# Optimization experiments

Measured on AMD Instinct MI355X. Metric: run time of the kernel, lower is better.

## Reference

```python
import jax, jax.numpy as jnp
import numpy as np
import math

N_AGENTS = 16

def _mlp2(x, W1, b1, W2, b2):
    # tanh on first layer only, matching the torch module
    return jnp.tanh(x @ W1 + b1) @ W2 + b2

def setup_inputs() -> dict:
    key = jax.random.key(0)
    ks = jax.random.split(key, 24)
    B, N, A, IN, D = 2048, N_AGENTS, 32, 128, 128
    NODES = B * N
    s = 0.05
    inp = {
        "obs": jax.random.normal(ks[0], (NODES, IN), jnp.float32),
        "policies": jax.random.uniform(ks[1], (NODES, A), jnp.float32),
        "actions": jax.random.uniform(ks[2], (NODES, A), jnp.float32),
        "weights": jax.random.uniform(ks[3], (1,), jnp.float32),
        "noise": jax.random.normal(ks[4], (NODES, N, A), jnp.float32) * 0.1,
        "Wk1": jax.random.normal(ks[5], (IN, 32), jnp.float32) * s,
        "bk1": jnp.zeros((32,), jnp.float32),
        "Wk2": jax.random.normal(ks[6], (32, D), jnp.float32) * s,
        "bk2": jnp.zeros((D,), jnp.float32),
        "Wq1": jax.random.normal(ks[7], (IN, 32), jnp.float32) * s,
        "bq1": jnp.zeros((32,), jnp.float32),
        "Wq2": jax.random.normal(ks[8], (32, D), jnp.float32) * s,
        "bq2": jnp.zeros((D,), jnp.float32),
        "Wv1": jax.random.normal(ks[9], (IN, 32), jnp.float32) * s,
        "bv1": jnp.zeros((32,), jnp.float32),
        "Wv2": jax.random.normal(ks[10], (32, D), jnp.float32) * s,
        "bv2": jnp.zeros((D,), jnp.float32),
        "Wval": jax.random.normal(ks[11], (D + A, 1), jnp.float32) * s,
        "bval": jnp.zeros((1,), jnp.float32),
    }
    return inp

def reference(obs, policies, actions, weights, noise,
              Wk1, bk1, Wk2, bk2, Wq1, bq1, Wq2, bq2, Wv1, bv1, Wv2, bv2,
              Wval, bval):
    N = N_AGENTS
    NODES, _ = obs.shape
    B = NODES // N
    A = policies.shape[-1]
    D = Wk2.shape[1]

    # ---- SoftAttentionInput: graph soft attention over complete N-agent graphs
    k = _mlp2(obs, Wk1, bk1, Wk2, bk2).reshape(B, N, D)
    q = _mlp2(obs, Wq1, bq1, Wq2, bq2).reshape(B, N, D)
    v = _mlp2(obs, Wv1, bv1, Wv2, bv2).reshape(B, N, D)
    # score for receiver i from sender j: key[j] . query[i]
    scores = jnp.einsum('bjd,bid->bij', k, q) / math.sqrt(D)
    alpha = jax.nn.softmax(scores, axis=-1)               # softmax over senders j
    obs_proc = jnp.einsum('bij,bjd->bid', alpha, v)       # [B,N,D]

    # ---- SoftAttentionWeight: PRD mixing of policies and noisy actions
    pi = policies.reshape(B, N, A)
    act = actions.reshape(B, N, A)
    w = weights                                           # scalar mixing weight, shape (1,)
    # z[b,i,k] = w*act[b,k] + (1-w)*pi[b,k] + noise (mailbox of receiver i)
    z = w * act[:, None, :, :] + (1.0 - w) * pi[:, None, :, :] + noise.reshape(B, N, N, A)
    # place_policies construction: z_final[b,i,j,k] = pi[b,k] if k==j else z[b,i,k];
    # mean over k  =>  (pi[b,j] - z[b,i,j] + sum_k z[b,i,k]) / N
    z_sum = jnp.sum(z, axis=2)                            # [B,N,A]
    z_mix = (pi[:, None, :, :] - z + z_sum[:, :, None, :]) / N  # [B,i,j,A]

    obs_b = jnp.broadcast_to(obs_proc[:, None, :, :], (B, N, N, D))  # [b,i,j] = obs_proc[b,j]
    obs_final = jnp.concatenate([obs_b, z_mix], axis=-1).reshape(B * N, N, D + A)

    # ---- ValueNetwork
    x = obs_final @ Wval + bval                           # [B*N, N, 1]
    weights_preproc = alpha.reshape(B * N, N, 1)
    return x, weights_preproc
```

## Files before the change

kernel.cpp:

```cpp
#include <hip/hip_runtime.h>

typedef __attribute__((ext_vector_type(8))) short bf16x8;
typedef __attribute__((ext_vector_type(4))) float f32x4;

__device__ __forceinline__ unsigned short f2bf(float f){
  union { float f; unsigned int u; } v; v.f = f;
  unsigned int u = v.u;
  return (unsigned short)((u + 0x7FFFu + ((u >> 16) & 1u)) >> 16);
}

__device__ __forceinline__ float fast_tanh(float x){
  x = fminf(15.f, fmaxf(-15.f, x));
  float e = __expf(2.f * x);
  return (e - 1.f) / (e + 1.f);
}

__device__ __forceinline__ float dot128(const float* __restrict__ a,
                                        const float* __restrict__ b){
  float s = 0.f;
  for (int c = 0; c < 128; c += 4){
    float4 x = *(const float4*)(a + c);
    float4 y = *(const float4*)(b + c);
    s += x.x*y.x + x.y*y.y + x.z*y.z + x.w*y.w;
  }
  return s;
}

#define GRPSUM(x) { x += __shfl_xor(x, 1); x += __shfl_xor(x, 2); \
                    x += __shfl_xor(x, 4); x += __shfl_xor(x, 8); }

__global__ __launch_bounds__(64) void k0_kernel(
    const float* __restrict__ Wk1, const float* __restrict__ Wq1, const float* __restrict__ Wv1,
    const float* __restrict__ Wk2, const float* __restrict__ bk2,
    const float* __restrict__ Wq2, const float* __restrict__ bq2,
    const float* __restrict__ Wv2, const float* __restrict__ bv2,
    const float* __restrict__ Wval, float* __restrict__ ws)
{
  const int tid = blockIdx.x * 64 + threadIdx.x;
  const float rs = 0.08838834764831845f;
  unsigned short* bp = (unsigned short*)ws;
  unsigned short* b2 = (unsigned short*)(ws + 6144);

  if (tid < 1536){
    const int e = tid & 7, l = (tid >> 3) & 63, tt = tid >> 9;
    const int g = (l >> 4) * 8 + e;
    float val = 0.f;
    if (tt < 2){
      const int h = (l & 15) + tt * 16;
      val = rs * dot128(Wk2 + h * 128, Wq2 + g * 128);
    } else if ((l & 15) == 0){
      val = rs * dot128(Wq2 + g * 128, bk2);
    }
    b2[tid] = f2bf(val);
  } else if (tid < 1600){
    const int h = tid - 1536;
    if (h < 32) ws[6912 + h] = rs * dot128(Wk2 + h * 128, bq2);
    else        ws[6944 + (h - 32)] = dot128(Wv2 + (h - 32) * 128, Wval);
  } else if (tid == 1600){
    ws[6976] = rs * dot128(bk2, bq2);
  } else if (tid == 1601){
    ws[6977] = dot128(bv2, Wval);
  }

  for (int idx = tid; idx < 12288; idx += 4096){
    const int e  = idx & 7;
    const int l  = (idx >> 3) & 63;
    const int kc = (idx >> 9) & 3;
    const int nt = (idx >> 11) & 1;
    const int m  = idx >> 12;
    const float* W1 = (m == 0) ? Wk1 : ((m == 1) ? Wq1 : Wv1);
    const int krow = kc * 32 + (l >> 4) * 8 + e;
    const int col  = nt * 16 + (l & 15);
    bp[idx] = f2bf(W1[krow * 32 + col]);
  }
}

__global__ __launch_bounds__(256) void k1_kernel(
    const float* __restrict__ obs, const float* __restrict__ noise,
    const float* __restrict__ bk1p, const float* __restrict__ bq1p, const float* __restrict__ bv1p,
    const float* __restrict__ Wval, const float* __restrict__ ws,
    float* __restrict__ out_x, float* __restrict__ out_alpha,
    float* __restrict__ ws_ov, int BA)
{
  __shared__ __align__(16) unsigned short hk_s[4][512];
  __shared__ __align__(16) unsigned short hq_s[4][512];
  __shared__ __align__(16) unsigned short tq_s[4][512];
  __shared__ __align__(16) float rql_s[4][16];
  __shared__ __align__(16) float vvl_s[4][16];
  __shared__ float nvw[256];

  const int t = threadIdx.x;

  if ((int)blockIdx.x >= BA){
    const int b = blockIdx.x - BA;
    const int q = t & 7;
    const float4 wv4 = *(const float4*)(Wval + 128 + q * 4);
    const float* nb = noise + (size_t)b * 8192 + (t >> 3) * 32 + q * 4;
#pragma unroll
    for (int p = 0; p < 8; p++){
      float4 n4 = *(const float4*)(nb + p * 1024);
      float s = n4.x*wv4.x + n4.y*wv4.y + n4.z*wv4.z + n4.w*wv4.w;
      s += __shfl_xor(s, 1); s += __shfl_xor(s, 2); s += __shfl_xor(s, 4);
      if (q == 0) nvw[p * 32 + (t >> 3)] = s;
    }
    __syncthreads();
    out_x[(size_t)b * 256 + t] = nvw[t];
    return;
  }

  const int wid = t >> 6, l = t & 63;
  const int b = blockIdx.x * 4 + wid;
  const int li = l & 15, gp = l >> 4;

  const float* orow = obs + (size_t)(b * 16 + li) * 128 + gp * 8;
  bf16x8 afr[4];
#pragma unroll
  for (int kc = 0; kc < 4; kc++){
    float4 x0 = *(const float4*)(orow + kc * 32);
    float4 x1 = *(const float4*)(orow + kc * 32 + 4);
    bf16x8 a;
    a[0]=(short)f2bf(x0.x); a[1]=(short)f2bf(x0.y); a[2]=(short)f2bf(x0.z); a[3]=(short)f2bf(x0.w);
    a[4]=(short)f2bf(x1.x); a[5]=(short)f2bf(x1.y); a[6]=(short)f2bf(x1.z); a[7]=(short)f2bf(x1.w);
    afr[kc] = a;
  }
  const bf16x8* bp  = (const bf16x8*)ws;
  const bf16x8* b2p = (const bf16x8*)(ws + 6144);
  const bf16x8 b20 = b2p[l], b21 = b2p[64 + l], b22 = b2p[128 + l];
  const float u0 = ws[6912 + li], u1 = ws[6928 + li];
  const float wv0 = ws[6944 + li], wv1 = ws[6960 + li];
  const float ccv = ws[6976], cvv = ws[6977];
  const float bk0 = bk1p[li], bk1v = bk1p[16 + li];
  const float bq0 = bq1p[li], bq1v = bq1p[16 + li];
  const float bv0 = bv1p[li], bv1v = bv1p[16 + li];

  f32x4 acc[6];
#pragma unroll
  for (int mt = 0; mt < 6; mt++){ f32x4 z = {0.f,0.f,0.f,0.f}; acc[mt] = z; }
#pragma unroll
  for (int mt = 0; mt < 6; mt++){
#pragma unroll
    for (int kc = 0; kc < 4; kc++)
      acc[mt] = __builtin_amdgcn_mfma_f32_16x16x32_bf16(afr[kc], bp[(mt*4+kc)*64 + l], acc[mt], 0, 0, 0);
  }

  unsigned short* hkb = hk_s[wid];
  unsigned short* hqb = hq_s[wid];
#pragma unroll
  for (int tile = 0; tile < 2; tile++){
    const float bk_ = tile ? bk1v : bk0;
    const float bq_ = tile ? bq1v : bq0;
    f32x4 ck = acc[tile], cq = acc[2 + tile];
#pragma unroll
    for (int r = 0; r < 4; r++){
      hkb[(gp*4+r)*32 + tile*16 + li] = f2bf(fast_tanh(ck[r] + bk_));
      hqb[(gp*4+r)*32 + tile*16 + li] = f2bf(fast_tanh(cq[r] + bq_));
    }
  }

  {
    f32x4 c0 = acc[4], c1 = acc[5];
    float vp0 = wv0*fast_tanh(c0[0]+bv0) + wv1*fast_tanh(c1[0]+bv1v);
    float vp1 = wv0*fast_tanh(c0[1]+bv0) + wv1*fast_tanh(c1[1]+bv1v);
    float vp2 = wv0*fast_tanh(c0[2]+bv0) + wv1*fast_tanh(c1[2]+bv1v);
    float vp3 = wv0*fast_tanh(c0[3]+bv0) + wv1*fast_tanh(c1[3]+bv1v);
    GRPSUM(vp0); GRPSUM(vp1); GRPSUM(vp2); GRPSUM(vp3);
    if (li == 0){
      float4 vq; vq.x = vp0+cvv; vq.y = vp1+cvv; vq.z = vp2+cvv; vq.w = vp3+cvv;
      *(float4*)&vvl_s[wid][gp*4] = vq;
    }
  }

  const bf16x8 aq = *(const bf16x8*)(hqb + li*32 + gp*8);
  f32x4 cu0 = {u0,u0,u0,u0}, cu1 = {u1,u1,u1,u1}, cu2 = {ccv,ccv,ccv,ccv};
  f32x4 tq0 = __builtin_amdgcn_mfma_f32_16x16x32_bf16(aq, b20, cu0, 0, 0, 0);
  f32x4 tq1 = __builtin_amdgcn_mfma_f32_16x16x32_bf16(aq, b21, cu1, 0, 0, 0);
  f32x4 rqt = __builtin_amdgcn_mfma_f32_16x16x32_bf16(aq, b22, cu2, 0, 0, 0);
  if (li == 0){
    float4 rv; rv.x = rqt[0]; rv.y = rqt[1]; rv.z = rqt[2]; rv.w = rqt[3];
    *(float4*)&rql_s[wid][gp*4] = rv;
  }
  unsigned short* tqb = tq_s[wid];
#pragma unroll
  for (int r = 0; r < 4; r++){
    tqb[(gp*4+r)*32 + li]      = f2bf(tq0[r]);
    tqb[(gp*4+r)*32 + 16 + li] = f2bf(tq1[r]);
  }

  const bf16x8 ak = *(const bf16x8*)(hkb + li*32 + gp*8);
  const bf16x8 bt = *(const bf16x8*)(tqb + li*32 + gp*8);
  f32x4 zz = {0.f,0.f,0.f,0.f};
  f32x4 S = __builtin_amdgcn_mfma_f32_16x16x32_bf16(ak, bt, zz, 0, 0, 0);
  const float rc = rql_s[wid][li];
  float s0 = S[0]+rc, s1 = S[1]+rc, s2 = S[2]+rc, s3 = S[3]+rc;

  float mx = fmaxf(fmaxf(s0, s1), fmaxf(s2, s3));
  mx = fmaxf(mx, __shfl_xor(mx, 16)); mx = fmaxf(mx, __shfl_xor(mx, 32));
  float e0 = __expf(s0-mx), e1 = __expf(s1-mx), e2 = __expf(s2-mx), e3 = __expf(s3-mx);
  float sm = e0+e1+e2+e3;
  sm += __shfl_xor(sm, 16); sm += __shfl_xor(sm, 32);
  const float inv = 1.f / sm;
  const float a0 = e0*inv, a1 = e1*inv, a2 = e2*inv, a3 = e3*inv;

  float* aT = (float*)tqb;
  { float4 av4; av4.x = a0; av4.y = a1; av4.z = a2; av4.w = a3;
    *(float4*)&aT[li*16 + gp*4] = av4; }
  { float4 o4 = *(const float4*)&aT[l*4];
    *(float4*)(out_alpha + (size_t)b*256 + l*4) = o4; }

  float4 vq4 = *(const float4*)&vvl_s[wid][gp*4];
  float ovp = a0*vq4.x + a1*vq4.y + a2*vq4.z + a3*vq4.w;
  ovp += __shfl_xor(ovp, 16); ovp += __shfl_xor(ovp, 32);
  if (l < 16) ws_ov[(size_t)b*16 + l] = ovp;
}

__global__ __launch_bounds__(256) void kc_kernel(
    const float* __restrict__ policies, const float* __restrict__ actions,
    const float* __restrict__ weights, const float* __restrict__ Wval,
    const float* __restrict__ bval, const float* __restrict__ ws_ov,
    float* __restrict__ out_x)
{
  __shared__ float pv_l[16], av_l[16];
  const int b = blockIdx.x, t = threadIdx.x;
  const float w = weights[0];
  {
    const int j = t >> 4; const int a0 = (t & 15) * 2;
    const float wa = Wval[128 + a0], wb = Wval[129 + a0];
    const float* pp = policies + ((size_t)(b * 16 + j)) * 32 + a0;
    const float* ap = actions  + ((size_t)(b * 16 + j)) * 32 + a0;
    float p = pp[0]*wa + pp[1]*wb;
    float a = ap[0]*wa + ap[1]*wb;
    GRPSUM(p); GRPSUM(a);
    if ((t & 15) == 0){ pv_l[j] = p; av_l[j] = a; }
  }
  __syncthreads();
  const int j = t & 15;
  const float pv = pv_l[j], av = av_l[j];
  const float nv = out_x[(size_t)b * 256 + t];
  const float zval = w * av + (1.f - w) * pv + nv;
  float zs = zval;
  GRPSUM(zs);
  out_x[(size_t)b * 256 + t] = ws_ov[(size_t)b * 16 + j] + (pv - zval + zs) * 0.0625f + bval[0];
}

extern "C" void kernel_launch(void* const* d_in, const int* in_sizes, int n_in,
                              void* d_out, int out_size, void* d_ws, size_t ws_size,
                              hipStream_t stream)
{
  const float* obs      = (const float*)d_in[0];
  const float* policies = (const float*)d_in[1];
  const float* actions  = (const float*)d_in[2];
  const float* weights  = (const float*)d_in[3];
  const float* noise    = (const float*)d_in[4];
  const float* Wk1  = (const float*)d_in[5];
  const float* bk1  = (const float*)d_in[6];
  const float* Wk2  = (const float*)d_in[7];
  const float* bk2  = (const float*)d_in[8];
  const float* Wq1  = (const float*)d_in[9];
  const float* bq1  = (const float*)d_in[10];
  const float* Wq2  = (const float*)d_in[11];
  const float* bq2  = (const float*)d_in[12];
  const float* Wv1  = (const float*)d_in[13];
  const float* bv1  = (const float*)d_in[14];
  const float* Wv2  = (const float*)d_in[15];
  const float* bv2  = (const float*)d_in[16];
  const float* Wval = (const float*)d_in[17];
  const float* bval = (const float*)d_in[18];

  float* out = (float*)d_out;
  float* ws  = (float*)d_ws;
  float* ws_ov = ws + 7168;

  const int NODES = in_sizes[0] / 128;
  const int B = NODES / 16;
  const int BA = B / 4;

  float* out_x     = out;
  float* out_alpha = out + (size_t)NODES * 16;

  hipLaunchKernelGGL(k0_kernel, dim3(64), dim3(64), 0, stream,
                     Wk1, Wq1, Wv1, Wk2, bk2, Wq2, bq2, Wv2, bv2, Wval, ws);
  hipLaunchKernelGGL(k1_kernel, dim3(BA + B), dim3(256), 0, stream,
                     obs, noise, bk1, bq1, bv1, Wval, ws,
                     out_x, out_alpha, ws_ov, BA);
  hipLaunchKernelGGL(kc_kernel, dim3(B), dim3(256), 0, stream,
                     policies, actions, weights, Wval, bval, ws_ov, out_x);
}
```

Before: 31.36 us.

## Fuse noise projection and PRD mixing into the attention kernel

Merges the separate noise-projection blocks and the final mixing kernel into the attention kernel. Each wave now handles one batch end to end: it streams that batch's noise in four software-pipelined register chunks interleaved with the MFMA work, computes the policy and action projections, and writes out_x directly. This drops one kernel launch and the global round trips through out_x and ws_ov. In exchange, register pressure is much higher (two 8-float4 noise buffers) and the grid falls to B/4 blocks, with launch bounds raised to ask for 2 blocks per CU.

```diff
diff --git a/kernel.cpp b/kernel.cpp
--- a/kernel.cpp
+++ b/kernel.cpp
@@ -75,54 +75,53 @@
   }
 }
 
-__global__ __launch_bounds__(256) void k1_kernel(
-    const float* __restrict__ obs, const float* __restrict__ noise,
+__global__ __launch_bounds__(256, 2) void fused_kernel(
+    const float* __restrict__ obs,
+    const float* __restrict__ policies, const float* __restrict__ actions,
+    const float* __restrict__ noise, const float* __restrict__ weights,
     const float* __restrict__ bk1p, const float* __restrict__ bq1p, const float* __restrict__ bv1p,
-    const float* __restrict__ Wval, const float* __restrict__ ws,
-    float* __restrict__ out_x, float* __restrict__ out_alpha,
-    float* __restrict__ ws_ov, int BA)
+    const float* __restrict__ Wval, const float* __restrict__ bval,
+    const float* __restrict__ ws,
+    float* __restrict__ out_x, float* __restrict__ out_alpha)
 {
   __shared__ __align__(16) unsigned short hk_s[4][512];
   __shared__ __align__(16) unsigned short hq_s[4][512];
   __shared__ __align__(16) unsigned short tq_s[4][512];
   __shared__ __align__(16) float rql_s[4][16];
   __shared__ __align__(16) float vvl_s[4][16];
-  __shared__ float nvw[256];
+  __shared__ __align__(16) float nvw_s[4][256];
+  __shared__ __align__(16) float pvl_s[4][16], avl_s[4][16], ovl_s[4][16];
 
   const int t = threadIdx.x;
-
-  if ((int)blockIdx.x >= BA){
-    const int b = blockIdx.x - BA;
-    const int q = t & 7;
-    const float4 wv4 = *(const float4*)(Wval + 128 + q * 4);
-    const float* nb = noise + (size_t)b * 8192 + (t >> 3) * 32 + q * 4;
-#pragma unroll
-    for (int p = 0; p < 8; p++){
-      float4 n4 = *(const float4*)(nb + p * 1024);
-      float s = n4.x*wv4.x + n4.y*wv4.y + n4.z*wv4.z + n4.w*wv4.w;
-      s += __shfl_xor(s, 1); s += __shfl_xor(s, 2); s += __shfl_xor(s, 4);
-      if (q == 0) nvw[p * 32 + (t >> 3)] = s;
-    }
-    __syncthreads();
-    out_x[(size_t)b * 256 + t] = nvw[t];
-    return;
-  }
-
   const int wid = t >> 6, l = t & 63;
   const int b = blockIdx.x * 4 + wid;
   const int li = l & 15, gp = l >> 4;
 
   const float* orow = obs + (size_t)(b * 16 + li) * 128 + gp * 8;
-  bf16x8 afr[4];
+  float4 ob[8];
 #pragma unroll
   for (int kc = 0; kc < 4; kc++){
-    float4 x0 = *(const float4*)(orow + kc * 32);
-    float4 x1 = *(const float4*)(orow + kc * 32 + 4);
-    bf16x8 a;
-    a[0]=(short)f2bf(x0.x); a[1]=(short)f2bf(x0.y); a[2]=(short)f2bf(x0.z); a[3]=(short)f2bf(x0.w);
-    a[4]=(short)f2bf(x1.x); a[5]=(short)f2bf(x1.y); a[6]=(short)f2bf(x1.z); a[7]=(short)f2bf(x1.w);
-    afr[kc] = a;
-  }
+    ob[kc * 2]     = *(const float4*)(orow + kc * 32);
+    ob[kc * 2 + 1] = *(const float4*)(orow + kc * 32 + 4);
+  }
+
+  const int q8 = l & 7, r8 = l >> 3;
+  const float* nb = noise + (size_t)b * 8192 + r8 * 32 + q8 * 4;
+  float4 nzA[8], nzB[8];
+#pragma unroll
+  for (int p = 0; p < 8; p++) nzA[p] = *(const float4*)(nb + p * 256);
+
+  const int jp = l >> 2, seg = l & 3;
+  const float* pp = policies + (size_t)(b * 16 + jp) * 32 + seg * 8;
+  const float* ap = actions  + (size_t)(b * 16 + jp) * 32 + seg * 8;
+  float4 pA0 = *(const float4*)(pp);
+  float4 pA1 = *(const float4*)(pp + 4);
+  float4 aA0 = *(const float4*)(ap);
+  float4 aA1 = *(const float4*)(ap + 4);
+  const float4 wpa = *(const float4*)(Wval + 128 + seg * 8);
+  const float4 wpb = *(const float4*)(Wval + 132 + seg * 8);
+  const float4 wv4 = *(const float4*)(Wval + 128 + q8 * 4);
+
   const bf16x8* bp  = (const bf16x8*)ws;
   const bf16x8* b2p = (const bf16x8*)(ws + 6144);
   const bf16x8 b20 = b2p[l], b21 = b2p[64 + l], b22 = b2p[128 + l];
@@ -132,7 +131,19 @@
   const float bk0 = bk1p[li], bk1v = bk1p[16 + li];
   const float bq0 = bq1p[li], bq1v = bq1p[16 + li];
   const float bv0 = bv1p[li], bv1v = bv1p[16 + li];
-
+  const float wscal = weights[0];
+  const float bvs = bval[0];
+
+  bf16x8 afr[4];
+#pragma unroll
+  for (int kc = 0; kc < 4; kc++){
+    bf16x8 a;
+    a[0]=(short)f2bf(ob[kc*2].x); a[1]=(short)f2bf(ob[kc*2].y);
+    a[2]=(short)f2bf(ob[kc*2].z); a[3]=(short)f2bf(ob[kc*2].w);
+    a[4]=(short)f2bf(ob[kc*2+1].x); a[5]=(short)f2bf(ob[kc*2+1].y);
+    a[6]=(short)f2bf(ob[kc*2+1].z); a[7]=(short)f2bf(ob[kc*2+1].w);
+    afr[kc] = a;
+  }
   f32x4 acc[6];
 #pragma unroll
   for (int mt = 0; mt < 6; mt++){ f32x4 z = {0.f,0.f,0.f,0.f}; acc[mt] = z; }
@@ -170,6 +181,18 @@
     }
   }
 
+#pragma unroll
+  for (int p = 0; p < 8; p++) nzB[p] = *(const float4*)(nb + 2048 + p * 256);
+  float* nvw = nvw_s[wid];
+#pragma unroll
+  for (int p = 0; p < 8; p++){
+    float s = nzA[p].x*wv4.x + nzA[p].y*wv4.y + nzA[p].z*wv4.z + nzA[p].w*wv4.w;
+    s += __shfl_xor(s, 1); s += __shfl_xor(s, 2); s += __shfl_xor(s, 4);
+    if (q8 == 0) nvw[p * 8 + r8] = s;
+  }
+#pragma unroll
+  for (int p = 0; p < 8; p++) nzA[p] = *(const float4*)(nb + 4096 + p * 256);
+
   const bf16x8 aq = *(const bf16x8*)(hqb + li*32 + gp*8);
   f32x4 cu0 = {u0,u0,u0,u0}, cu1 = {u1,u1,u1,u1}, cu2 = {ccv,ccv,ccv,ccv};
   f32x4 tq0 = __builtin_amdgcn_mfma_f32_16x16x32_bf16(aq, b20, cu0, 0, 0, 0);
@@ -210,36 +233,61 @@
   float4 vq4 = *(const float4*)&vvl_s[wid][gp*4];
   float ovp = a0*vq4.x + a1*vq4.y + a2*vq4.z + a3*vq4.w;
   ovp += __shfl_xor(ovp, 16); ovp += __shfl_xor(ovp, 32);
-  if (l < 16) ws_ov[(size_t)b*16 + l] = ovp;
-}
-
-__global__ __launch_bounds__(256) void kc_kernel(
-    const float* __restrict__ policies, const float* __restrict__ actions,
-    const float* __restrict__ weights, const float* __restrict__ Wval,
-    const float* __restrict__ bval, const float* __restrict__ ws_ov,
-    float* __restrict__ out_x)
-{
-  __shared__ float pv_l[16], av_l[16];
-  const int b = blockIdx.x, t = threadIdx.x;
-  const float w = weights[0];
+  if (l < 16) ovl_s[wid][li] = ovp;
+
+#pragma unroll
+  for (int p = 0; p < 8; p++){
+    float s = nzB[p].x*wv4.x + nzB[p].y*wv4.y + nzB[p].z*wv4.z + nzB[p].w*wv4.w;
+    s += __shfl_xor(s, 1); s += __shfl_xor(s, 2); s += __shfl_xor(s, 4);
+    if (q8 == 0) nvw[64 + p * 8 + r8] = s;
+  }
+#pragma unroll
+  for (int p = 0; p < 8; p++) nzB[p] = *(const float4*)(nb + 6144 + p * 256);
+
   {
-    const int j = t >> 4; const int a0 = (t & 15) * 2;
-    const float wa = Wval[128 + a0], wb = Wval[129 + a0];
-    const float* pp = policies + ((size_t)(b * 16 + j)) * 32 + a0;
-    const float* ap = actions  + ((size_t)(b * 16 + j)) * 32 + a0;
-    float p = pp[0]*wa + pp[1]*wb;
-    float a = ap[0]*wa + ap[1]*wb;
-    GRPSUM(p); GRPSUM(a);
-    if ((t & 15) == 0){ pv_l[j] = p; av_l[j] = a; }
-  }
-  __syncthreads();
-  const int j = t & 15;
-  const float pv = pv_l[j], av = av_l[j];
-  const float nv = out_x[(size_t)b * 256 + t];
-  const float zval = w * av + (1.f - w) * pv + nv;
-  float zs = zval;
-  GRPSUM(zs);
-  out_x[(size_t)b * 256 + t] = ws_ov[(size_t)b * 16 + j] + (pv - zval + zs) * 0.0625f + bval[0];
+    float pvv = pA0.x*wpa.x + pA0.y*wpa.y + pA0.z*wpa.z + pA0.w*wpa.w
+              + pA1.x*wpb.x + pA1.y*wpb.y + pA1.z*wpb.z + pA1.w*wpb.w;
+    float avv = aA0.x*wpa.x + aA0.y*wpa.y + aA0.z*wpa.z + aA0.w*wpa.w
+              + aA1.x*wpb.x + aA1.y*wpb.y + aA1.z*wpb.z + aA1.w*wpb.w;
+    pvv += __shfl_xor(pvv, 1); pvv += __shfl_xor(pvv, 2);
+    avv += __shfl_xor(avv, 1); avv += __shfl_xor(avv, 2);
+    if (seg == 0){ pvl_s[wid][jp] = pvv; avl_s[wid][jp] = avv; }
+  }
+
+#pragma unroll
+  for (int p = 0; p < 8; p++){
+    float s = nzA[p].x*wv4.x + nzA[p].y*wv4.y + nzA[p].z*wv4.z + nzA[p].w*wv4.w;
+    s += __shfl_xor(s, 1); s += __shfl_xor(s, 2); s += __shfl_xor(s, 4);
+    if (q8 == 0) nvw[128 + p * 8 + r8] = s;
+  }
+#pragma unroll
+  for (int p = 0; p < 8; p++){
+    float s = nzB[p].x*wv4.x + nzB[p].y*wv4.y + nzB[p].z*wv4.z + nzB[p].w*wv4.w;
+    s += __shfl_xor(s, 1); s += __shfl_xor(s, 2); s += __shfl_xor(s, 4);
+    if (q8 == 0) nvw[192 + p * 8 + r8] = s;
+  }
+
+  {
+    const int j0 = (l & 3) * 4;
+    const int ii = l >> 2;
+    float4 pv4 = *(const float4*)&pvl_s[wid][j0];
+    float4 av4 = *(const float4*)&avl_s[wid][j0];
+    float4 ov4 = *(const float4*)&ovl_s[wid][j0];
+    float4 nv4 = *(const float4*)&nvw[ii * 16 + j0];
+    const float om = 1.f - wscal;
+    float z0 = wscal * av4.x + om * pv4.x + nv4.x;
+    float z1 = wscal * av4.y + om * pv4.y + nv4.y;
+    float z2 = wscal * av4.z + om * pv4.z + nv4.z;
+    float z3 = wscal * av4.w + om * pv4.w + nv4.w;
+    float zs = z0 + z1 + z2 + z3;
+    zs += __shfl_xor(zs, 1); zs += __shfl_xor(zs, 2);
+    float4 o;
+    o.x = ov4.x + (pv4.x - z0 + zs) * 0.0625f + bvs;
+    o.y = ov4.y + (pv4.y - z1 + zs) * 0.0625f + bvs;
+    o.z = ov4.z + (pv4.z - z2 + zs) * 0.0625f + bvs;
+    o.w = ov4.w + (pv4.w - z3 + zs) * 0.0625f + bvs;
+    *(float4*)(out_x + (size_t)b * 256 + l * 4) = o;
+  }
 }
 
 extern "C" void kernel_launch(void* const* d_in, const int* in_sizes, int n_in,
@@ -268,20 +316,17 @@
 
   float* out = (float*)d_out;
   float* ws  = (float*)d_ws;
-  float* ws_ov = ws + 7168;
 
   const int NODES = in_sizes[0] / 128;
   const int B = NODES / 16;
-  const int BA = B / 4;
 
   float* out_x     = out;
   float* out_alpha = out + (size_t)NODES * 16;
 
   hipLaunchKernelGGL(k0_kernel, dim3(64), dim3(64), 0, stream,
                      Wk1, Wq1, Wv1, Wk2, bk2, Wq2, bq2, Wv2, bv2, Wval, ws);
-  hipLaunchKernelGGL(k1_kernel, dim3(BA + B), dim3(256), 0, stream,
-                     obs, noise, bk1, bq1, bv1, Wval, ws,
-                     out_x, out_alpha, ws_ov, BA);
-  hipLaunchKernelGGL(kc_kernel, dim3(B), dim3(256), 0, stream,
-                     policies, actions, weights, Wval, bval, ws_ov, out_x);
-}
+  hipLaunchKernelGGL(fused_kernel, dim3(B / 4), dim3(256), 0, stream,
+                     obs, policies, actions, noise, weights,
+                     bk1, bq1, bv1, Wval, bval, ws,
+                     out_x, out_alpha);
+}
```

After: 30.80 us. About the same (-1.8%).
